# Optimization experiments

Hardware: AMD Instinct MI355X
Metric: run time of the kernel (lower is better)

Reference implementation:

```python
import jax, jax.numpy as jnp
import numpy as np

CODEBOOK_SIZE = 8192
DIM = 256
COMMITMENT_COST = 0.25


def setup_inputs() -> dict:
    key = jax.random.key(0)
    k1, k2 = jax.random.split(key)
    z = jax.random.normal(k1, (8, DIM, 1024), dtype=jnp.float32)
    # nn.init.uniform_(codebook.weight, -1/K, 1/K)
    bound = 1.0 / CODEBOOK_SIZE
    codebook = jax.random.uniform(k2, (CODEBOOK_SIZE, DIM), dtype=jnp.float32,
                                  minval=-bound, maxval=bound)
    return {"z": z, "codebook": codebook}


def reference(z, codebook):
    B, D, T = z.shape
    z_perm = jnp.transpose(z, (0, 2, 1)).reshape(B * T, D)  # (BT, D)
    # ||z||^2 - 2 z.c + ||c||^2  -> (BT, K)
    distances = (jnp.sum(z_perm * z_perm, axis=1, keepdims=True)
                 - 2.0 * (z_perm @ codebook.T)
                 + jnp.sum(codebook * codebook, axis=1)[None, :])
    indices = jnp.argmin(distances, axis=1)          # (BT,)
    z_q_flat = codebook[indices]                     # (BT, D)
    z_q = jnp.transpose(z_q_flat.reshape(B, T, D), (0, 2, 1))  # (B, D, T)

    codebook_loss = jnp.mean((z_q - jax.lax.stop_gradient(z)) ** 2)
    commitment_loss = COMMITMENT_COST * jnp.mean((jax.lax.stop_gradient(z_q) - z) ** 2)
    loss = codebook_loss + commitment_loss

    # straight-through estimator
    z_q_st = z + jax.lax.stop_gradient(z_q - z)
    return z_q_st, indices.reshape(B, T), loss
```

## Files before the change

### kernel.cpp

```cpp
#include <hip/hip_runtime.h>

#define DD   256
#define TT   1024
#define BT   8192
#define KK   8192
#define ZQ_SIZE 2097152

#define FLT_INF 3.402823466e38f

typedef __attribute__((ext_vector_type(8))) short short8;
typedef __attribute__((ext_vector_type(4))) float f32x4;

#define A2_B    0u
#define B2_B    12582912u
#define AN_B    25165824u
#define CN_B    25198592u
#define KEY_B   25231360u
#define ACC_B   25296896u

static __device__ __forceinline__ unsigned short f2bf(float x) {
    unsigned int u = __float_as_uint(x);
    return (unsigned short)((u + 0x7FFF + ((u >> 16) & 1)) >> 16);
}
static __device__ __forceinline__ float bf2f(unsigned short h) {
    return __uint_as_float(((unsigned int)h) << 16);
}
static __device__ __forceinline__ void split3(float x, unsigned short& h,
                                              unsigned short& m, unsigned short& l) {
    h = f2bf(x);
    float r1 = x - bf2f(h);
    m = f2bf(r1);
    l = f2bf(r1 - bf2f(m));
}

static __device__ __forceinline__ void gld16(const void* g, const void* l) {
    __builtin_amdgcn_global_load_lds(
        (const __attribute__((address_space(1))) unsigned int*)g,
        (__attribute__((address_space(3))) unsigned int*)l, 16, 0, 0);
}

__global__ __launch_bounds__(256) void vq_prep(const float* __restrict__ z,
                                               const float* __restrict__ cb,
                                               float* __restrict__ An,
                                               unsigned short* __restrict__ A2,
                                               unsigned short* __restrict__ B2,
                                               float* __restrict__ Cn,
                                               unsigned long long* __restrict__ keys,
                                               float* __restrict__ lacc) {
    __shared__ float T[64][257];
    int tid = threadIdx.x;
    if (blockIdx.x < 32) {
        int g = blockIdx.x * 256 + tid;
        int b = g >> 10, t = g & 1023;
        const float* zp = z + (size_t)b * (DD * TT) + t;
        float s = 0.f;
        #pragma unroll 8
        for (int d = 0; d < DD; ++d) {
            float v = zp[d * TT];
            float v2 = v * v;
            s = s + v2;
        }
        An[g] = s;
        keys[g] = ~0ull;
        if (g == 0) *lacc = 0.f;
    } else if (blockIdx.x < 32 + 2048) {
        int g = (blockIdx.x - 32) * 256 + tid;
        int code = g >> 6, d4 = (g & 63) * 4;
        float4 v = *(const float4*)&cb[(size_t)code * DD + d4];
        unsigned short h[4], m[4], l[4];
        split3(v.x, h[0], m[0], l[0]);
        split3(v.y, h[1], m[1], l[1]);
        split3(v.z, h[2], m[2], l[2]);
        split3(v.w, h[3], m[3], l[3]);
        int ng = code >> 4;
        int lane = ((d4 >> 3) & 3) * 16 + (code & 15);
        int kk = d4 >> 5;
        int jb = d4 & 7;
        size_t base = (size_t)((ng * 3) * 8 + kk) * 512 + lane * 8 + jb;
        *(ushort4*)&B2[base]        = make_ushort4(h[0], h[1], h[2], h[3]);
        *(ushort4*)&B2[base + 4096] = make_ushort4(m[0], m[1], m[2], m[3]);
        *(ushort4*)&B2[base + 8192] = make_ushort4(l[0], l[1], l[2], l[3]);
        float s = v.x * v.x + v.y * v.y + v.z * v.z + v.w * v.w;
        #pragma unroll
        for (int off = 32; off; off >>= 1) s += __shfl_down(s, off, 64);
        if ((tid & 63) == 0) Cn[code] = s;
    } else {
        int blk = blockIdx.x - 2080;
        int b = blk >> 4;
        int t0 = (blk & 15) * 64;
        #pragma unroll
        for (int it = 0; it < 16; ++it) {
            int d = it * 16 + (tid >> 4);
            int t4 = (tid & 15) * 4;
            float4 v = *(const float4*)&z[(size_t)b * (DD * TT) + (size_t)d * TT + t0 + t4];
            T[t4 + 0][d] = v.x; T[t4 + 1][d] = v.y; T[t4 + 2][d] = v.z; T[t4 + 3][d] = v.w;
        }
        __syncthreads();
        int r = tid >> 2, q = tid & 3;
        int t = b * 1024 + t0 + r;
        int gA = t >> 4, ml = t & 15;
        #pragma unroll
        for (int dd = 0; dd < 16; ++dd) {
            int d = dd * 16 + q * 4;
            unsigned short h[4], m[4], l[4];
            #pragma unroll
            for (int c = 0; c < 4; ++c) split3(T[r][d + c], h[c], m[c], l[c]);
            int kk = d >> 5, quad = (d >> 3) & 3, jb = d & 7;
            size_t base = (size_t)((gA * 3) * 8 + kk) * 512 + (quad * 16 + ml) * 8 + jb;
            *(ushort4*)&A2[base]        = make_ushort4(h[0], h[1], h[2], h[3]);
            *(ushort4*)&A2[base + 4096] = make_ushort4(m[0], m[1], m[2], m[3]);
            *(ushort4*)&A2[base + 8192] = make_ushort4(l[0], l[1], l[2], l[3]);
        }
    }
}

__global__ __launch_bounds__(256, 2) void vq_scores(const unsigned short* __restrict__ A2,
                                                    const unsigned short* __restrict__ B2,
                                                    const float* __restrict__ An,
                                                    const float* __restrict__ Cn,
                                                    unsigned long long* __restrict__ keys) {
    __shared__ __attribute__((aligned(16))) unsigned short Bl[2][12288];

    int bid = blockIdx.x;
    int g = bid >> 6, sl = bid & 63;
    int mt = (g >> 3) * 8 + (sl >> 3);
    int nt = (g & 7) * 8 + (sl & 7);
    const int token0 = mt * 256, code0 = nt * 128;

    const int wid = threadIdx.x >> 6, lane = threadIdx.x & 63;
    const int quad = lane >> 4, col = lane & 15;

    int sidx[6]; size_t soff[6];
    #pragma unroll
    for (int n = 0; n < 6; ++n) {
        int idx = wid * 6 + n;
        int p = idx >> 3, ngl = idx & 7;
        sidx[n] = idx * 512;
        soff[n] = (size_t)(((nt * 8 + ngl) * 3 + p) * 8) * 512 + lane * 8;
    }

    f32x4 acc[4][8];
    #pragma unroll
    for (int i = 0; i < 4; ++i)
        #pragma unroll
        for (int j = 0; j < 8; ++j) acc[i][j] = (f32x4){0.f, 0.f, 0.f, 0.f};

    #pragma unroll
    for (int n = 0; n < 6; ++n)
        gld16(B2 + soff[n], &Bl[0][sidx[n]]);

    const int gm0 = (token0 >> 4) + wid * 4;
    const int PP[6] = {0, 1, 2, 0, 1, 0};
    const int QQ[6] = {0, 0, 0, 1, 1, 2};

    for (int kk = 0; kk < 8; ++kk) {
        __syncthreads();
        if (kk < 7) {
            #pragma unroll
            for (int n = 0; n < 6; ++n)
                gld16(B2 + soff[n] + (size_t)(kk + 1) * 512, &Bl[(kk + 1) & 1][sidx[n]]);
        }
        const unsigned short* B = Bl[kk & 1];
        short8 bf[8];
        #pragma unroll
        for (int t = 0; t < 6; ++t) {
            const int p = PP[t], q = QQ[t];
            if (t == 0 || q != QQ[t - 1]) {
                #pragma unroll
                for (int j = 0; j < 8; ++j)
                    bf[j] = *(const short8*)&B[(q * 8 + j) * 512 + lane * 8];
            }
            short8 af[4];
            #pragma unroll
            for (int i = 0; i < 4; ++i)
                af[i] = *(const short8*)&A2[(size_t)(((gm0 + i) * 3 + p) * 8 + kk) * 512
                                            + lane * 8];
            #pragma unroll
            for (int i = 0; i < 4; ++i)
                #pragma unroll
                for (int j = 0; j < 8; ++j)
                    acc[i][j] = __builtin_amdgcn_mfma_f32_16x16x32_bf16(
                        af[i], bf[j], acc[i][j], 0, 0, 0);
        }
    }

    float cn[8]; int cidx[8];
    #pragma unroll
    for (int j = 0; j < 8; ++j) {
        cidx[j] = code0 + j * 16 + col;
        cn[j] = Cn[cidx[j]];
    }
    #pragma unroll
    for (int i = 0; i < 4; ++i) {
        #pragma unroll
        for (int r = 0; r < 4; ++r) {
            int token = token0 + wid * 64 + i * 16 + quad * 4 + r;
            float Ai = An[token];
            float bv = FLT_INF; int bi = 0;
            #pragma unroll
            for (int j = 0; j < 8; ++j) {
                float d1 = fmaf(-2.f, acc[i][j][r], Ai);
                float dist = d1 + cn[j];
                if (dist < bv) { bv = dist; bi = cidx[j]; }
            }
            #pragma unroll
            for (int off = 8; off; off >>= 1) {
                float ov = __shfl_down(bv, off, 16);
                int   oi = __shfl_down(bi, off, 16);
                if (ov < bv || (ov == bv && oi < bi)) { bv = ov; bi = oi; }
            }
            if (col == 0) {
                unsigned long long key =
                    ((unsigned long long)__float_as_uint(bv) << 32) | (unsigned)bi;
                atomicMin(&keys[token], key);
            }
        }
    }
}

__global__ __launch_bounds__(256) void vq_gather(const float* __restrict__ z,
                                                 const float* __restrict__ cb,
                                                 const unsigned long long* __restrict__ keys,
                                                 float* __restrict__ out,
                                                 float* __restrict__ out_idx,
                                                 float* __restrict__ loss_acc) {
    int e4 = blockIdx.x * 256 + threadIdx.x;
    int t4 = e4 & 255;
    int rest = e4 >> 8;
    int d = rest & 255;
    int b = rest >> 8;
    int gbase = b * 1024 + t4 * 4;

    const int* klo = (const int*)keys;
    int i0 = klo[(size_t)(gbase + 0) * 2];
    int i1 = klo[(size_t)(gbase + 1) * 2];
    int i2 = klo[(size_t)(gbase + 2) * 2];
    int i3 = klo[(size_t)(gbase + 3) * 2];
    if (d == 0) {
        out_idx[gbase + 0] = (float)i0;
        out_idx[gbase + 1] = (float)i1;
        out_idx[gbase + 2] = (float)i2;
        out_idx[gbase + 3] = (float)i3;
    }

    float4 zv = *(const float4*)&z[(size_t)e4 * 4];
    float q0 = cb[(size_t)i0 * DD + d];
    float q1 = cb[(size_t)i1 * DD + d];
    float q2 = cb[(size_t)i2 * DD + d];
    float q3 = cb[(size_t)i3 * DD + d];

    float d0 = q0 - zv.x, d1 = q1 - zv.y, d2 = q2 - zv.z, d3 = q3 - zv.w;
    float4 o;
    o.x = zv.x + d0; o.y = zv.y + d1; o.z = zv.z + d2; o.w = zv.w + d3;
    *(float4*)&out[(size_t)e4 * 4] = o;

    float s = d0 * d0 + d1 * d1 + d2 * d2 + d3 * d3;
    #pragma unroll
    for (int off = 32; off; off >>= 1) s += __shfl_down(s, off, 64);
    __shared__ float wsum[4];
    if ((threadIdx.x & 63) == 0) wsum[threadIdx.x >> 6] = s;
    __syncthreads();
    if (threadIdx.x == 0)
        atomicAdd(loss_acc, wsum[0] + wsum[1] + wsum[2] + wsum[3]);
}

__global__ void vq_loss(const float* __restrict__ loss_acc, float* __restrict__ out_loss) {
    *out_loss = 1.25f * (*loss_acc) / 2097152.f;
}

extern "C" void kernel_launch(void* const* d_in, const int* in_sizes, int n_in,
                              void* d_out, int out_size, void* d_ws, size_t ws_size,
                              hipStream_t stream) {
    const float* z  = (const float*)d_in[0];
    const float* cb = (const float*)d_in[1];
    float* out = (float*)d_out;
    char*  w   = (char*)d_ws;

    unsigned short* A2 = (unsigned short*)(w + A2_B);
    unsigned short* B2 = (unsigned short*)(w + B2_B);
    float* An = (float*)(w + AN_B);
    float* Cn = (float*)(w + CN_B);
    unsigned long long* keys = (unsigned long long*)(w + KEY_B);
    float* lacc = (float*)(w + ACC_B);

    vq_prep   <<<32 + 2048 + 128, 256, 0, stream>>>(z, cb, An, A2, B2, Cn, keys, lacc);
    vq_scores <<<2048, 256, 0, stream>>>(A2, B2, An, Cn, keys);
    vq_gather <<<ZQ_SIZE / 1024, 256, 0, stream>>>(z, cb, keys, out, out + ZQ_SIZE, lacc);
    vq_loss   <<<1, 1, 0, stream>>>(lacc, out + ZQ_SIZE + BT);
}
```

Baseline: 269.2 us.

## Shrink score tile to 128x128 with 2x2 wave grid and fuse norms into prep

```diff
diff --git a/kernel.cpp b/kernel.cpp
--- a/kernel.cpp
+++ b/kernel.cpp
@@ -49,23 +49,13 @@
                                                float* __restrict__ lacc) {
     __shared__ float T[64][257];
     int tid = threadIdx.x;
-    if (blockIdx.x < 32) {
+    if (blockIdx.x < 2048) {
         int g = blockIdx.x * 256 + tid;
-        int b = g >> 10, t = g & 1023;
-        const float* zp = z + (size_t)b * (DD * TT) + t;
-        float s = 0.f;
-        #pragma unroll 8
-        for (int d = 0; d < DD; ++d) {
-            float v = zp[d * TT];
-            float v2 = v * v;
-            s = s + v2;
-        }
-        An[g] = s;
-        keys[g] = ~0ull;
-        if (g == 0) *lacc = 0.f;
-    } else if (blockIdx.x < 32 + 2048) {
-        int g = (blockIdx.x - 32) * 256 + tid;
         int code = g >> 6, d4 = (g & 63) * 4;
+        if (d4 == 0) {
+            keys[code] = ~0ull;
+            if (code == 0) *lacc = 0.f;
+        }
         float4 v = *(const float4*)&cb[(size_t)code * DD + d4];
         unsigned short h[4], m[4], l[4];
         split3(v.x, h[0], m[0], l[0]);
@@ -85,7 +75,7 @@
         for (int off = 32; off; off >>= 1) s += __shfl_down(s, off, 64);
         if ((tid & 63) == 0) Cn[code] = s;
     } else {
-        int blk = blockIdx.x - 2080;
+        int blk = blockIdx.x - 2048;
         int b = blk >> 4;
         int t0 = (blk & 15) * 64;
         #pragma unroll
@@ -99,22 +89,30 @@
         int r = tid >> 2, q = tid & 3;
         int t = b * 1024 + t0 + r;
         int gA = t >> 4, ml = t & 15;
+        float s = 0.f;
         #pragma unroll
         for (int dd = 0; dd < 16; ++dd) {
             int d = dd * 16 + q * 4;
+            float v0 = T[r][d], v1 = T[r][d + 1], v2 = T[r][d + 2], v3 = T[r][d + 3];
             unsigned short h[4], m[4], l[4];
-            #pragma unroll
-            for (int c = 0; c < 4; ++c) split3(T[r][d + c], h[c], m[c], l[c]);
+            split3(v0, h[0], m[0], l[0]);
+            split3(v1, h[1], m[1], l[1]);
+            split3(v2, h[2], m[2], l[2]);
+            split3(v3, h[3], m[3], l[3]);
+            s = s + v0 * v0; s = s + v1 * v1; s = s + v2 * v2; s = s + v3 * v3;
             int kk = d >> 5, quad = (d >> 3) & 3, jb = d & 7;
             size_t base = (size_t)((gA * 3) * 8 + kk) * 512 + (quad * 16 + ml) * 8 + jb;
             *(ushort4*)&A2[base]        = make_ushort4(h[0], h[1], h[2], h[3]);
             *(ushort4*)&A2[base + 4096] = make_ushort4(m[0], m[1], m[2], m[3]);
             *(ushort4*)&A2[base + 8192] = make_ushort4(l[0], l[1], l[2], l[3]);
         }
-    }
-}
-
-__global__ __launch_bounds__(256, 2) void vq_scores(const unsigned short* __restrict__ A2,
+        s += __shfl_down(s, 1, 4);
+        s += __shfl_down(s, 2, 4);
+        if (q == 0) An[t] = s;
+    }
+}
+
+__global__ __launch_bounds__(256, 3) void vq_scores(const unsigned short* __restrict__ A2,
                                                     const unsigned short* __restrict__ B2,
                                                     const float* __restrict__ An,
                                                     const float* __restrict__ Cn,
@@ -125,10 +123,11 @@
     int g = bid >> 6, sl = bid & 63;
     int mt = (g >> 3) * 8 + (sl >> 3);
     int nt = (g & 7) * 8 + (sl & 7);
-    const int token0 = mt * 256, code0 = nt * 128;
+    const int token0 = mt * 128, code0 = nt * 128;
 
     const int wid = threadIdx.x >> 6, lane = threadIdx.x & 63;
     const int quad = lane >> 4, col = lane & 15;
+    const int m0w = (wid >> 1) * 64, n0w = (wid & 1) * 64;
 
     int sidx[6]; size_t soff[6];
     #pragma unroll
@@ -139,17 +138,18 @@
         soff[n] = (size_t)(((nt * 8 + ngl) * 3 + p) * 8) * 512 + lane * 8;
     }
 
-    f32x4 acc[4][8];
+    f32x4 acc[4][4];
     #pragma unroll
     for (int i = 0; i < 4; ++i)
         #pragma unroll
-        for (int j = 0; j < 8; ++j) acc[i][j] = (f32x4){0.f, 0.f, 0.f, 0.f};
+        for (int j = 0; j < 4; ++j) acc[i][j] = (f32x4){0.f, 0.f, 0.f, 0.f};
 
     #pragma unroll
     for (int n = 0; n < 6; ++n)
         gld16(B2 + soff[n], &Bl[0][sidx[n]]);
 
-    const int gm0 = (token0 >> 4) + wid * 4;
+    const int gm0 = (token0 >> 4) + (wid >> 1) * 4;
+    const int ng0 = n0w >> 4;
     const int PP[6] = {0, 1, 2, 0, 1, 0};
     const int QQ[6] = {0, 0, 0, 1, 1, 2};
 
@@ -161,14 +161,14 @@
                 gld16(B2 + soff[n] + (size_t)(kk + 1) * 512, &Bl[(kk + 1) & 1][sidx[n]]);
         }
         const unsigned short* B = Bl[kk & 1];
-        short8 bf[8];
+        short8 bf[4];
         #pragma unroll
         for (int t = 0; t < 6; ++t) {
             const int p = PP[t], q = QQ[t];
             if (t == 0 || q != QQ[t - 1]) {
                 #pragma unroll
-                for (int j = 0; j < 8; ++j)
-                    bf[j] = *(const short8*)&B[(q * 8 + j) * 512 + lane * 8];
+                for (int j = 0; j < 4; ++j)
+                    bf[j] = *(const short8*)&B[(q * 8 + ng0 + j) * 512 + lane * 8];
             }
             short8 af[4];
             #pragma unroll
@@ -178,27 +178,27 @@
             #pragma unroll
             for (int i = 0; i < 4; ++i)
                 #pragma unroll
-                for (int j = 0; j < 8; ++j)
+                for (int j = 0; j < 4; ++j)
                     acc[i][j] = __builtin_amdgcn_mfma_f32_16x16x32_bf16(
                         af[i], bf[j], acc[i][j], 0, 0, 0);
         }
     }
 
-    float cn[8]; int cidx[8];
-    #pragma unroll
-    for (int j = 0; j < 8; ++j) {
-        cidx[j] = code0 + j * 16 + col;
+    float cn[4]; int cidx[4];
+    #pragma unroll
+    for (int j = 0; j < 4; ++j) {
+        cidx[j] = code0 + n0w + j * 16 + col;
         cn[j] = Cn[cidx[j]];
     }
     #pragma unroll
     for (int i = 0; i < 4; ++i) {
         #pragma unroll
         for (int r = 0; r < 4; ++r) {
-            int token = token0 + wid * 64 + i * 16 + quad * 4 + r;
+            int token = token0 + m0w + i * 16 + quad * 4 + r;
             float Ai = An[token];
             float bv = FLT_INF; int bi = 0;
             #pragma unroll
-            for (int j = 0; j < 8; ++j) {
+            for (int j = 0; j < 4; ++j) {
                 float d1 = fmaf(-2.f, acc[i][j][r], Ai);
                 float dist = d1 + cn[j];
                 if (dist < bv) { bv = dist; bi = cidx[j]; }
@@ -283,8 +283,8 @@
     unsigned long long* keys = (unsigned long long*)(w + KEY_B);
     float* lacc = (float*)(w + ACC_B);
 
-    vq_prep   <<<32 + 2048 + 128, 256, 0, stream>>>(z, cb, An, A2, B2, Cn, keys, lacc);
-    vq_scores <<<2048, 256, 0, stream>>>(A2, B2, An, Cn, keys);
+    vq_prep   <<<2048 + 128, 256, 0, stream>>>(z, cb, An, A2, B2, Cn, keys, lacc);
+    vq_scores <<<4096, 256, 0, stream>>>(A2, B2, An, Cn, keys);
     vq_gather <<<ZQ_SIZE / 1024, 256, 0, stream>>>(z, cb, keys, out, out + ZQ_SIZE, lacc);
     vq_loss   <<<1, 1, 0, stream>>>(lacc, out + ZQ_SIZE + BT);
 }
```

After: 293.9 us. 1.09x slower.
